# Performance work log

Hardware: AMD Instinct MI355X
Metric: run time of the kernel (lower is better)

Reference implementation:

```python
import jax, jax.numpy as jnp
import numpy as np

B, H, S, D = 4, 16, 2048, 64


def setup_inputs() -> dict:
    key = jax.random.key(0)
    kq, kk, kv = jax.random.split(key, 3)
    q = jax.random.normal(kq, (B, H, S, D), dtype=jnp.float32)
    k = jax.random.normal(kk, (B, H, S, D), dtype=jnp.float32)
    v = jax.random.normal(kv, (B, H, S, D), dtype=jnp.float32)
    return {"q": q, "k": k, "v": v}


def reference(q, k, v):
    # scores: [B, H, S_q, S_k]
    scale = 1.0 / jnp.sqrt(jnp.asarray(q.shape[-1], q.dtype))
    scores = jnp.einsum("bhqd,bhkd->bhqk", q, k) * scale
    attn = jax.nn.softmax(scores, axis=-1)
    # dropout p=0.0 -> identity
    return jnp.einsum("bhqk,bhkd->bhqd", attn, v)
```

## Files before the change

### kernel.cpp

```cpp
#include <hip/hip_runtime.h>


#define S_LEN 2048
#define D_LEN 64
#define QT    128
#define TK    64
#define THREADS 256
#define KSTR  72
#define NT    (S_LEN / TK)

typedef __attribute__((ext_vector_type(8)))  short bf16x8;
typedef __attribute__((ext_vector_type(16))) float f32x16;

#if __has_builtin(__builtin_amdgcn_exp2f)
#define FAST_EXP2(x) __builtin_amdgcn_exp2f(x)
#else
#define FAST_EXP2(x) __expf((x) * 0.69314718055994531f)
#endif

__device__ __forceinline__ unsigned pk2(float a, float b) {
    unsigned r;
    asm("v_cvt_pk_bf16_f32 %0, %1, %2" : "=v"(r) : "v"(a), "v"(b));
    return r;
}

__device__ __forceinline__ void pl32(unsigned& a, unsigned& b) {
    asm("v_permlane32_swap_b32 %0, %1" : "+v"(a), "+v"(b));
}

__global__ __launch_bounds__(THREADS, 4)
void attn_mfma32(const float* __restrict__ qg,
                 const float* __restrict__ kg,
                 const float* __restrict__ vg,
                 float* __restrict__ og)
{
    __shared__ alignas(16) unsigned short Ks[2][TK * KSTR];
    __shared__ alignas(16) unsigned short Vt[2][D_LEN * KSTR];

    const int tid  = threadIdx.x;
    const int w    = tid >> 6;
    const int lane = tid & 63;
    const int q31  = lane & 31;
    const int hi   = lane >> 5;

    const int swz   = (blockIdx.x & 7) * 128 + (blockIdx.x >> 3);
    const int bh    = swz >> 4;
    const int qblk  = swz & 15;
    const int qrow0 = qblk * QT + w * 32;

    const float* kbase = kg + (size_t)bh * S_LEN * D_LEN;
    const float* vbase = vg + (size_t)bh * S_LEN * D_LEN;

    const float c = 0.125f * 1.4426950408889634f;
    bf16x8 qf[4];
    {
        const float* qp = qg + ((size_t)bh * S_LEN + qrow0 + q31) * D_LEN + hi * 8;
#pragma unroll
        for (int kf = 0; kf < 4; ++kf) {
            float4 a = ((const float4*)(qp + kf * 16))[0];
            float4 b = ((const float4*)(qp + kf * 16))[1];
            uint4 u = make_uint4(pk2(a.x * c, a.y * c), pk2(a.z * c, a.w * c),
                                 pk2(b.x * c, b.y * c), pk2(b.z * c, b.w * c));
            qf[kf] = __builtin_bit_cast(bf16x8, u);
        }
    }

    f32x16 o0, o1;
#pragma unroll
    for (int i = 0; i < 16; ++i) { o0[i] = 0.f; o1[i] = 0.f; }
    float lsum = 0.f;

    const int skey = tid >> 2;
    const int sc   = tid & 3;
    const float4* kptr = (const float4*)kbase + (size_t)skey * 16 + sc * 4;
    const float* vptr = vbase + (size_t)(w * 16) * D_LEN + lane;

    float4 kreg[4];
    float  vreg[16];
#pragma unroll
    for (int i = 0; i < 4; ++i) kreg[i] = kptr[i];
#pragma unroll
    for (int r = 0; r < 16; ++r) vreg[r] = vptr[r * 64];

    auto stage = [&](int buf) {
        uint4 u0 = make_uint4(pk2(kreg[0].x, kreg[0].y), pk2(kreg[0].z, kreg[0].w),
                              pk2(kreg[1].x, kreg[1].y), pk2(kreg[1].z, kreg[1].w));
        uint4 u1 = make_uint4(pk2(kreg[2].x, kreg[2].y), pk2(kreg[2].z, kreg[2].w),
                              pk2(kreg[3].x, kreg[3].y), pk2(kreg[3].z, kreg[3].w));
        *(uint4*)&Ks[buf][skey * KSTR + sc * 16]     = u0;
        *(uint4*)&Ks[buf][skey * KSTR + sc * 16 + 8] = u1;
        uint4 v0 = make_uint4(pk2(vreg[0], vreg[1]),   pk2(vreg[2], vreg[3]),
                              pk2(vreg[4], vreg[5]),   pk2(vreg[6], vreg[7]));
        uint4 v1 = make_uint4(pk2(vreg[8], vreg[9]),   pk2(vreg[10], vreg[11]),
                              pk2(vreg[12], vreg[13]), pk2(vreg[14], vreg[15]));
        *(uint4*)&Vt[buf][lane * KSTR + w * 16]     = v0;
        *(uint4*)&Vt[buf][lane * KSTR + w * 16 + 8] = v1;
    };

    stage(0);
    __syncthreads();

    for (int t = 0; t < NT; ++t) {
        const int cur = t & 1;

        if (t + 1 < NT) {
            const float4* kn = kptr + (size_t)(t + 1) * (TK * 16);
#pragma unroll
            for (int i = 0; i < 4; ++i) kreg[i] = kn[i];
            const float* vn = vptr + (size_t)(t + 1) * (TK * D_LEN);
#pragma unroll
            for (int r = 0; r < 16; ++r) vreg[r] = vn[r * 64];
        }

#pragma unroll
        for (int kt = 0; kt < 2; ++kt) {
            f32x16 s;
#pragma unroll
            for (int i = 0; i < 16; ++i) s[i] = 0.f;
#pragma unroll
            for (int kf = 0; kf < 4; ++kf) {
                bf16x8 ka = *(const bf16x8*)&Ks[cur][(kt * 32 + q31) * KSTR + kf * 16 + hi * 8];
                s = __builtin_amdgcn_mfma_f32_32x32x16_bf16(ka, qf[kf], s, 0, 0, 0);
            }
#pragma unroll
            for (int f = 0; f < 2; ++f) {
                const int b = f * 8;
                float p0 = FAST_EXP2(s[b + 0]), p1 = FAST_EXP2(s[b + 1]);
                float p2 = FAST_EXP2(s[b + 2]), p3 = FAST_EXP2(s[b + 3]);
                float p4 = FAST_EXP2(s[b + 4]), p5 = FAST_EXP2(s[b + 5]);
                float p6 = FAST_EXP2(s[b + 6]), p7 = FAST_EXP2(s[b + 7]);
                lsum += ((p0 + p1) + (p2 + p3)) + ((p4 + p5) + (p6 + p7));
                unsigned a0 = pk2(p0, p1), a1 = pk2(p4, p5);
                unsigned b0 = pk2(p2, p3), b1 = pk2(p6, p7);
                pl32(a0, a1);
                pl32(b0, b1);
                uint4 u = make_uint4(a0, b0, a1, b1);
                bf16x8 pb = __builtin_bit_cast(bf16x8, u);
                const int kq = kt * 2 + f;
                bf16x8 va0 = *(const bf16x8*)&Vt[cur][q31 * KSTR + kq * 16 + hi * 8];
                bf16x8 va1 = *(const bf16x8*)&Vt[cur][(32 + q31) * KSTR + kq * 16 + hi * 8];
                o0 = __builtin_amdgcn_mfma_f32_32x32x16_bf16(va0, pb, o0, 0, 0, 0);
                o1 = __builtin_amdgcn_mfma_f32_32x32x16_bf16(va1, pb, o1, 0, 0, 0);
            }
        }

        if (t + 1 < NT) {
            stage(cur ^ 1);
            __syncthreads();
        }
    }

    float l = lsum + __shfl_xor(lsum, 32);
    const float inv = 1.0f / l;
    float* ob = og + ((size_t)bh * S_LEN + qrow0 + q31) * D_LEN;
#pragma unroll
    for (int g = 0; g < 4; ++g) {
        float4 f0 = make_float4(o0[4 * g + 0] * inv, o0[4 * g + 1] * inv,
                                o0[4 * g + 2] * inv, o0[4 * g + 3] * inv);
        ((float4*)(ob + g * 8 + hi * 4))[0] = f0;
        float4 f1 = make_float4(o1[4 * g + 0] * inv, o1[4 * g + 1] * inv,
                                o1[4 * g + 2] * inv, o1[4 * g + 3] * inv);
        ((float4*)(ob + 32 + g * 8 + hi * 4))[0] = f1;
    }
}

extern "C" void kernel_launch(void* const* d_in, const int* in_sizes, int n_in,
                              void* d_out, int out_size, void* d_ws, size_t ws_size,
                              hipStream_t stream)
{
    const float* q = (const float*)d_in[0];
    const float* k = (const float*)d_in[1];
    const float* v = (const float*)d_in[2];
    float* out = (float*)d_out;

    dim3 grid(64 * (S_LEN / QT));
    dim3 block(THREADS);
    attn_mfma32<<<grid, block, 0, stream>>>(q, k, v, out);
}
```

Measured before the change: 209.8 us.

## Software-pipeline PV MFMAs one tile behind QK and softmax

Restructures the main loop so the P·V MFMAs for tile t-1 run at the start of iteration t, using P fragments and V operands held in registers from the previous iteration. QK^T MFMAs and exp for the current tile then follow, so matrix and transcendental work from different tiles can overlap. The PV block is wrapped in s_setprio to favour MFMA issue. V fragments are loaded into registers before the barrier, which raises register pressure (8 extra bf16x8 V values plus 4 P values) under a launch bound of 4 and may reduce occupancy or cause spills.

```diff
diff --git a/kernel.cpp b/kernel.cpp
--- a/kernel.cpp
+++ b/kernel.cpp
@@ -27,6 +27,48 @@
 __device__ __forceinline__ void pl32(unsigned& a, unsigned& b) {
     asm("v_permlane32_swap_b32 %0, %1" : "+v"(a), "+v"(b));
 }
+
+#define SMAX(S, B, POUT)                                                    \
+    {                                                                       \
+        float p0 = FAST_EXP2(S[(B) + 0]), p1 = FAST_EXP2(S[(B) + 1]);       \
+        float p2 = FAST_EXP2(S[(B) + 2]), p3 = FAST_EXP2(S[(B) + 3]);       \
+        float p4 = FAST_EXP2(S[(B) + 4]), p5 = FAST_EXP2(S[(B) + 5]);       \
+        float p6 = FAST_EXP2(S[(B) + 6]), p7 = FAST_EXP2(S[(B) + 7]);       \
+        lsum += ((p0 + p1) + (p2 + p3)) + ((p4 + p5) + (p6 + p7));          \
+        unsigned a0 = pk2(p0, p1), a1 = pk2(p4, p5);                        \
+        unsigned b0 = pk2(p2, p3), b1 = pk2(p6, p7);                        \
+        pl32(a0, a1);                                                       \
+        pl32(b0, b1);                                                       \
+        uint4 u = make_uint4(a0, b0, a1, b1);                               \
+        POUT = __builtin_bit_cast(bf16x8, u);                               \
+    }
+
+#define QK_TILE(KT, POUT0, POUT1)                                           \
+    {                                                                       \
+        f32x16 s;                                                           \
+        s = __builtin_amdgcn_mfma_f32_32x32x16_bf16(                        \
+            *(const bf16x8*)&Ks[cur][((KT)*32 + q31)*KSTR + 0*16 + hi*8],   \
+            qf0, (f32x16){0.f}, 0, 0, 0);                                   \
+        s = __builtin_amdgcn_mfma_f32_32x32x16_bf16(                        \
+            *(const bf16x8*)&Ks[cur][((KT)*32 + q31)*KSTR + 1*16 + hi*8],   \
+            qf1, s, 0, 0, 0);                                               \
+        s = __builtin_amdgcn_mfma_f32_32x32x16_bf16(                        \
+            *(const bf16x8*)&Ks[cur][((KT)*32 + q31)*KSTR + 2*16 + hi*8],   \
+            qf2, s, 0, 0, 0);                                               \
+        s = __builtin_amdgcn_mfma_f32_32x32x16_bf16(                        \
+            *(const bf16x8*)&Ks[cur][((KT)*32 + q31)*KSTR + 3*16 + hi*8],   \
+            qf3, s, 0, 0, 0);                                               \
+        SMAX(s, 0, POUT0);                                                  \
+        SMAX(s, 8, POUT1);                                                  \
+    }
+
+#define VLOAD(KQ, VA0, VA1)                                                 \
+    VA0 = *(const bf16x8*)&Vt[cur][q31*KSTR + (KQ)*16 + hi*8];              \
+    VA1 = *(const bf16x8*)&Vt[cur][(32 + q31)*KSTR + (KQ)*16 + hi*8];
+
+#define PVSTEP(VA0, VA1, PB)                                                \
+    o0 = __builtin_amdgcn_mfma_f32_32x32x16_bf16(VA0, PB, o0, 0, 0, 0);     \
+    o1 = __builtin_amdgcn_mfma_f32_32x32x16_bf16(VA1, PB, o1, 0, 0, 0);
 
 __global__ __launch_bounds__(THREADS, 4)
 void attn_mfma32(const float* __restrict__ qg,
@@ -52,17 +94,19 @@
     const float* vbase = vg + (size_t)bh * S_LEN * D_LEN;
 
     const float c = 0.125f * 1.4426950408889634f;
-    bf16x8 qf[4];
+    bf16x8 qf0, qf1, qf2, qf3;
     {
         const float* qp = qg + ((size_t)bh * S_LEN + qrow0 + q31) * D_LEN + hi * 8;
-#pragma unroll
-        for (int kf = 0; kf < 4; ++kf) {
-            float4 a = ((const float4*)(qp + kf * 16))[0];
-            float4 b = ((const float4*)(qp + kf * 16))[1];
-            uint4 u = make_uint4(pk2(a.x * c, a.y * c), pk2(a.z * c, a.w * c),
-                                 pk2(b.x * c, b.y * c), pk2(b.z * c, b.w * c));
-            qf[kf] = __builtin_bit_cast(bf16x8, u);
+#define QLOAD(KF, QF)                                                       \
+        {                                                                   \
+            float4 a = ((const float4*)(qp + (KF) * 16))[0];                \
+            float4 b = ((const float4*)(qp + (KF) * 16))[1];                \
+            uint4 u = make_uint4(pk2(a.x*c, a.y*c), pk2(a.z*c, a.w*c),      \
+                                 pk2(b.x*c, b.y*c), pk2(b.z*c, b.w*c));     \
+            QF = __builtin_bit_cast(bf16x8, u);                             \
         }
+        QLOAD(0, qf0) QLOAD(1, qf1) QLOAD(2, qf2) QLOAD(3, qf3)
+#undef QLOAD
     }
 
     f32x16 o0, o1;
@@ -100,9 +144,22 @@
     stage(0);
     __syncthreads();
 
+    bf16x8 pbv0, pbv1, pbv2, pbv3;
+    bf16x8 va00, va01, va02, va03;
+    bf16x8 va10, va11, va12, va13;
+
     for (int t = 0; t < NT; ++t) {
         const int cur = t & 1;
 
+        if (t > 0) {
+            __builtin_amdgcn_s_setprio(1);
+            PVSTEP(va00, va10, pbv0)
+            PVSTEP(va01, va11, pbv1)
+            PVSTEP(va02, va12, pbv2)
+            PVSTEP(va03, va13, pbv3)
+            __builtin_amdgcn_s_setprio(0);
+        }
+
         if (t + 1 < NT) {
             const float4* kn = kptr + (size_t)(t + 1) * (TK * 16);
 #pragma unroll
@@ -112,43 +169,22 @@
             for (int r = 0; r < 16; ++r) vreg[r] = vn[r * 64];
         }
 
-#pragma unroll
-        for (int kt = 0; kt < 2; ++kt) {
-            f32x16 s;
-#pragma unroll
-            for (int i = 0; i < 16; ++i) s[i] = 0.f;
-#pragma unroll
-            for (int kf = 0; kf < 4; ++kf) {
-                bf16x8 ka = *(const bf16x8*)&Ks[cur][(kt * 32 + q31) * KSTR + kf * 16 + hi * 8];
-                s = __builtin_amdgcn_mfma_f32_32x32x16_bf16(ka, qf[kf], s, 0, 0, 0);
-            }
-#pragma unroll
-            for (int f = 0; f < 2; ++f) {
-                const int b = f * 8;
-                float p0 = FAST_EXP2(s[b + 0]), p1 = FAST_EXP2(s[b + 1]);
-                float p2 = FAST_EXP2(s[b + 2]), p3 = FAST_EXP2(s[b + 3]);
-                float p4 = FAST_EXP2(s[b + 4]), p5 = FAST_EXP2(s[b + 5]);
-                float p6 = FAST_EXP2(s[b + 6]), p7 = FAST_EXP2(s[b + 7]);
-                lsum += ((p0 + p1) + (p2 + p3)) + ((p4 + p5) + (p6 + p7));
-                unsigned a0 = pk2(p0, p1), a1 = pk2(p4, p5);
-                unsigned b0 = pk2(p2, p3), b1 = pk2(p6, p7);
-                pl32(a0, a1);
-                pl32(b0, b1);
-                uint4 u = make_uint4(a0, b0, a1, b1);
-                bf16x8 pb = __builtin_bit_cast(bf16x8, u);
-                const int kq = kt * 2 + f;
-                bf16x8 va0 = *(const bf16x8*)&Vt[cur][q31 * KSTR + kq * 16 + hi * 8];
-                bf16x8 va1 = *(const bf16x8*)&Vt[cur][(32 + q31) * KSTR + kq * 16 + hi * 8];
-                o0 = __builtin_amdgcn_mfma_f32_32x32x16_bf16(va0, pb, o0, 0, 0, 0);
-                o1 = __builtin_amdgcn_mfma_f32_32x32x16_bf16(va1, pb, o1, 0, 0, 0);
-            }
-        }
-
-        if (t + 1 < NT) {
-            stage(cur ^ 1);
-            __syncthreads();
-        }
-    }
+        QK_TILE(0, pbv0, pbv1)
+        QK_TILE(1, pbv2, pbv3)
+
+        VLOAD(0, va00, va10)
+        VLOAD(1, va01, va11)
+        VLOAD(2, va02, va12)
+        VLOAD(3, va03, va13)
+
+        if (t + 1 < NT) stage(cur ^ 1);
+        __syncthreads();
+    }
+
+    PVSTEP(va00, va10, pbv0)
+    PVSTEP(va01, va11, pbv1)
+    PVSTEP(va02, va12, pbv2)
+    PVSTEP(va03, va13, pbv3)
 
     float l = lsum + __shfl_xor(lsum, 32);
     const float inv = 1.0f / l;
```

Result: slower. 220.7 us (+5.2%).
